# Kernel optimization log

Hardware: AMD Instinct MI355X
Metric: run time of the kernel (lower is better)

The kernel has to match this reference:

```python
import jax, jax.numpy as jnp
import numpy as np
from jax import lax

B, P, NB, NF, NC, R = 128, 2048, 2000, 250, 16, 128
LS = NB - NF  # number of simulated bins = len_bins_gensig - 1


def setup_inputs() -> dict:
    key = jax.random.key(0)
    ks = jax.random.split(key, 10)
    return {
        'batched_stim_spat': jax.random.normal(ks[0], (B, P), jnp.float32),
        'stim_time': jax.random.normal(ks[1], (NB,), jnp.float32),
        'batched_initial_spike_section': (jax.random.uniform(ks[2], (B, NF)) < 0.05).astype(jnp.float32),
        'batched_coupling_cells': (jax.random.uniform(ks[3], (B, NC, NB)) < 0.05).astype(jnp.float32),
        'spatial_filter': jax.random.normal(ks[4], (P,), jnp.float32) * 0.02,
        'spatial_bias': jnp.float32(-2.0),
        'stim_timecourse_filter': jax.random.normal(ks[5], (NF,), jnp.float32) * 0.1,
        'feedback_filter': jax.random.normal(ks[6], (NF,), jnp.float32) * 0.05 - 0.02,
        'coupling_filter': jax.random.normal(ks[7], (NC, NF), jnp.float32) * 0.05,
        'u': jax.random.uniform(ks[8], (LS, B, R), jnp.float32),
        'n_repeats': R,
    }


def _corr1d_valid(x, k):
    # torch F.conv1d is cross-correlation; lax conv is too (no kernel flip)
    # x: (n,), k: (m,) -> (n - m + 1,)
    out = lax.conv_general_dilated(x[None, None, :], k[None, None, :], (1,), 'VALID',
                                   dimension_numbers=('NCH', 'OIH', 'NCH'))
    return out[0, 0]


def reference(batched_stim_spat, stim_time, batched_initial_spike_section,
              batched_coupling_cells, spatial_filter, spatial_bias,
              stim_timecourse_filter, feedback_filter, coupling_filter, u, n_repeats):
    nf = stim_timecourse_filter.shape[0]

    # stimulus time component: (n_bins - nf + 1,)
    filt_time = _corr1d_valid(stim_time, stim_timecourse_filter)

    # spatial exp arg for separable linear-spatial GLM:
    # einsum('bpt,p->bt', stim_spat[:,:,None]*filt_time, spatial_filter)
    # factors into outer product of (stim_spat @ spatial_filter) and filt_time
    stim_gensig = (batched_stim_spat @ spatial_filter)[:, None] * filt_time[None, :] + spatial_bias  # (B, T)

    # coupling exp arg: conv1d over all coupled cells -> (B, T)
    coup = lax.conv_general_dilated(batched_coupling_cells, coupling_filter[None, :, :], (1,), 'VALID',
                                    dimension_numbers=('NCH', 'OIH', 'NCH'))[:, 0, :]

    gensig_piece = stim_gensig + coup  # (B, T) with T = n_bins - nf + 1
    len_sim = gensig_piece.shape[1] - 1

    # initial feedback window: last nf spike bins, broadcast over repeats
    batch = batched_stim_spat.shape[0]
    w0 = jnp.broadcast_to(batched_initial_spike_section[:, None, :], (batch, n_repeats, nf)) + 0.0

    def step(window, xs):
        g_t, u_t = xs  # (B,), (B, R)
        fb = jnp.einsum('brk,k->br', window, feedback_filter)
        g = g_t[:, None] + fb
        spike = (u_t < jax.nn.sigmoid(g)).astype(window.dtype)  # Bernoulli(sigmoid(g))
        window = jnp.concatenate([window[:, :, 1:], spike[:, :, None]], axis=2)
        return window, spike

    xs = (jnp.swapaxes(gensig_piece[:, :len_sim], 0, 1), u[:len_sim])  # ((LS,B), (LS,B,R))
    _, spikes = lax.scan(step, w0, xs)  # spikes: (LS, B, R)

    out = jnp.concatenate([w0, jnp.moveaxis(spikes, 0, 2)], axis=2)  # (B, R, n_bins)
    return out
```

## Files before the change

### kernel.cpp

```cpp
#include <hip/hip_runtime.h>
#include <math.h>

#define B_  128
#define P_  2048
#define NB_ 2000
#define NF_ 250
#define NC_ 16
#define R_  128
#define LS_ 1750
#define NT_ 1751
#define BR_ (B_ * R_)
#define H_  16
#define NBLK_ 110

typedef int v4i __attribute__((ext_vector_type(4)));

__device__ __forceinline__ unsigned csel32(unsigned a, unsigned b, unsigned long long m) {
    unsigned r;
    asm("v_cndmask_b32 %0, %1, %2, %3" : "=v"(r) : "v"(a), "v"(b), "s"(m));
    return r;
}

__device__ __forceinline__ double dsel2(double t, unsigned long long m) {
    long long tb = __double_as_longlong(t);
    int tlo = (int)tb, thi = (int)(tb >> 32);
    int rlo, rhi;
    asm("v_cndmask_b32 %0, 0, %2, %4\n\t"
        "v_cndmask_b32 %1, 0, %3, %4"
        : "=&v"(rlo), "=&v"(rhi)
        : "v"(tlo), "v"(thi), "s"(m));
    return __longlong_as_double(((long long)(unsigned)rlo) | ((long long)rhi << 32));
}

__device__ __forceinline__ double dand(double t, int m) {
    return __longlong_as_double(__double_as_longlong(t) & (long long)m);
}

__device__ __forceinline__ double fdiv_fast(double a, double b) {
    double r;
    asm("v_rcp_f64 %0, %1" : "=v"(r) : "v"(b));
    r = fma(fma(-b, r, 1.0), r, r);
    r = fma(fma(-b, r, 1.0), r, r);
    double q = a * r;
    q = fma(fma(-b, q, a), r, q);
    return q;
}

__device__ __forceinline__ double logit_fast(float uf) {
    double u = (double)uf;
    double v = 1.0 - u;
    double qd = fdiv_fast(u, v);
    long long bits = __double_as_longlong(qd);
    int e = (int)((bits >> 52) & 0x7FF) - 1023;
    double m = __longlong_as_double((bits & 0xFFFFFFFFFFFFFLL) | 0x3FF0000000000000LL);
    if (m > 1.4142135623730951) { m *= 0.5; e += 1; }
    double s = fdiv_fast(m - 1.0, m + 1.0);
    double z = s * s;
    double Q = fma(z, fma(z, fma(z, fma(z,
        0.09090909090909091, 0.1111111111111111),
        0.14285714285714285), 0.2), 0.3333333333333333);
    double logm = fma(2.0 * s, z * Q, 2.0 * s);
    return fma((double)e, 0.6931471805599453, logm);
}

__global__ __launch_bounds__(256) void k_pre(const float* __restrict__ st,
                                             const float* __restrict__ stf,
                                             const float* __restrict__ sp,
                                             const float* __restrict__ sf,
                                             double* __restrict__ ft,
                                             double* __restrict__ sdot) {
    if (blockIdx.x < 7) {
        int t = blockIdx.x * 256 + threadIdx.x;
        if (t >= NT_) return;
        double s = 0.0;
        for (int k = 0; k < NF_; ++k) s += (double)st[t + k] * (double)stf[k];
        ft[t] = s;
    } else {
        __shared__ double red[256];
        int b = blockIdx.x - 7;
        double s = 0.0;
        for (int p = threadIdx.x; p < P_; p += 256)
            s += (double)sp[(size_t)b * P_ + p] * (double)sf[p];
        red[threadIdx.x] = s;
        __syncthreads();
        for (int off = 128; off > 0; off >>= 1) {
            if (threadIdx.x < off) red[threadIdx.x] += red[threadIdx.x + off];
            __syncthreads();
        }
        if (threadIdx.x == 0) sdot[b] = red[0];
    }
}

__global__ __launch_bounds__(256) void k_coup(const float* __restrict__ cc,
                                              const float* __restrict__ cf,
                                              const double* __restrict__ sdot,
                                              const double* __restrict__ ft,
                                              const float* __restrict__ bias,
                                              double* __restrict__ gensig) {
    __shared__ __align__(16) float  ccs[NC_ * 512];
    __shared__ __align__(16) double cfs[NC_ * 256];
    __shared__ double red[3][64][4];
    int b = blockIdx.y, t0 = blockIdx.x * 256;
    int tid = threadIdx.x, lane = tid & 63, wv = tid >> 6;

    for (int idx = tid; idx < NC_ * 128; idx += 256) {
        int c = idx >> 7, j4 = (idx & 127) * 4, src = t0 + j4;
        const float* p = cc + ((size_t)b * NC_ + c) * NB_ + src;
        float4 v;
        if (src + 3 < NB_) v = *(const float4*)p;
        else {
            v.x = (src     < NB_) ? p[0] : 0.f;
            v.y = (src + 1 < NB_) ? p[1] : 0.f;
            v.z = (src + 2 < NB_) ? p[2] : 0.f;
            v.w = (src + 3 < NB_) ? p[3] : 0.f;
        }
        *(float4*)&ccs[c * 512 + j4] = v;
    }
    for (int idx = tid; idx < NC_ * 256; idx += 256) {
        int c = idx >> 8, k = idx & 255;
        cfs[idx] = (k < NF_) ? (double)cf[c * NF_ + k] : 0.0;
    }
    __syncthreads();

    double a0 = 0, a1 = 0, a2 = 0, a3 = 0;
    int base = lane * 4;
    for (int c = wv; c < NC_; c += 4) {
        const float*  row  = &ccs[c * 512];
        const double* crow = &cfs[c * 256];
        float4 cur = *(const float4*)&row[base];
        for (int k4 = 0; k4 < 252; k4 += 4) {
            float4 nxt = *(const float4*)&row[base + k4 + 4];
            double e0 = cur.x, e1 = cur.y, e2 = cur.z, e3 = cur.w;
            double e4 = nxt.x, e5 = nxt.y, e6 = nxt.z;
            double c0 = crow[k4], c1 = crow[k4 + 1], c2 = crow[k4 + 2], c3 = crow[k4 + 3];
            a0 += e0 * c0 + e1 * c1 + e2 * c2 + e3 * c3;
            a1 += e1 * c0 + e2 * c1 + e3 * c2 + e4 * c3;
            a2 += e2 * c0 + e3 * c1 + e4 * c2 + e5 * c3;
            a3 += e3 * c0 + e4 * c1 + e5 * c2 + e6 * c3;
            cur = nxt;
        }
    }
    if (wv > 0) {
        red[wv - 1][lane][0] = a0; red[wv - 1][lane][1] = a1;
        red[wv - 1][lane][2] = a2; red[wv - 1][lane][3] = a3;
    }
    __syncthreads();
    if (wv == 0) {
        a0 += red[0][lane][0] + red[1][lane][0] + red[2][lane][0];
        a1 += red[0][lane][1] + red[1][lane][1] + red[2][lane][1];
        a2 += red[0][lane][2] + red[1][lane][2] + red[2][lane][2];
        a3 += red[0][lane][3] + red[1][lane][3] + red[2][lane][3];
        double gb = (double)bias[0];
        double sd = sdot[b];
        double accs[4] = {a0, a1, a2, a3};
        int tb = t0 + base;
        for (int i = 0; i < 4; ++i) {
            int t = tb + i;
            if (t < LS_) gensig[(size_t)b * LS_ + t] = sd * ft[t] + gb + accs[i];
        }
    }
}

__global__ __launch_bounds__(512, 2) void k_scan(const double* __restrict__ gensig,
                                                 const float* __restrict__ u,
                                                 const float* __restrict__ iss,
                                                 const float* __restrict__ ff,
                                                 float* __restrict__ out) {
    __shared__ double farT_all[4][16 * 17];
    __shared__ double luring[2][4][4 * 64];
    int tid = threadIdx.x;
    int wv = tid >> 6, l = tid & 63;
    int swv = wv & 3;
    const bool isPrep = (wv >= 4);
    int gw = blockIdx.x * 4 + swv;
    int b = gw >> 3, rbase = (gw & 7) * 16;
    double* farT = &farT_all[swv][0];

    int lw = l & 15;
    int q  = l >> 4;
    int cn = l >> 2;
    int j  = l & 3;
    int jo = 16 + j;

    const unsigned long long COL0_ = 0x1111111111111111ull;
    const unsigned long long COL1_ = COL0_ << 1;
    const unsigned long long COL2_ = COL0_ << 2;
    const unsigned long long COL3_ = COL0_ << 3;
    const unsigned long long COL01_ = COL0_ | COL1_;

    const double* gs   = gensig + (size_t)b * LS_;
    const float*  up   = u + b * R_ + rbase + cn;
    float*        op   = out + ((size_t)(b * R_ + rbase + cn)) * NB_ + NF_;
    const float*  issb = iss + b * NF_;

    unsigned long long W0 = 0, W1 = 0, W2 = 0, W3 = 0;
    v4i Bf[4][6];
    double T1d = 0, T2d = 0, T3d = 0, T4d = 0, T5d = 0, T6d = 0;
    double tp7 = 0, tp8 = 0, tp9 = 0, tp10 = 0, tp11 = 0, tp12 = 0, tp13 = 0, tp14 = 0;
    double tp15 = 0;
    double thr0 = 0, thr1 = 0, thr2 = 0, thr3 = 0;
    double gprep = 0.0;
    float ur0 = 0.f, ur1 = 0.f, ur2 = 0.f, ur3 = 0.f;

    if (!isPrep) {
        for (int idx = l; idx < 16 * NF_; idx += 64) {
            int c = idx / NF_, k = idx - c * NF_;
            out[((size_t)(b * R_ + rbase + c)) * NB_ + k] = issb[k];
        }
        for (int k = 0; k < NF_; ++k) {
            unsigned long long bit = (issb[k] > 0.5f) ? 1ull : 0ull;
            if      (k <  64) W0 |= bit << k;
            else if (k < 128) W1 |= bit << (k - 64);
            else if (k < 192) W2 |= bit << (k - 128);
            else              W3 |= bit << (k - 192);
        }
        int Bword[4][6][4];
#pragma unroll
        for (int kc = 0; kc < 4; ++kc)
#pragma unroll
            for (int p = 0; p < 6; ++p)
#pragma unroll
                for (int w = 0; w < 4; ++w) Bword[kc][p][w] = 0;
#pragma unroll
        for (int kc = 0; kc < 4; ++kc) {
#pragma unroll
            for (int jj = 0; jj < 16; ++jj) {
                int k = kc * 64 + q * 16 + jj;
                int idx = k - lw;
                long long v = 0;
                if (idx >= 0 && idx < NF_)
                    v = __double2ll_rn((double)ff[idx] * 281474976710656.0);
#pragma unroll
                for (int p = 0; p < 6; ++p) {
                    int d = (int)((v + 128) & 255) - 128;
                    v = (v - (long long)d) >> 8;
                    Bword[kc][p][jj >> 2] |= (d & 255) << ((jj & 3) * 8);
                }
            }
        }
#pragma unroll
        for (int kc = 0; kc < 4; ++kc)
#pragma unroll
            for (int p = 0; p < 6; ++p) {
                v4i t; t.x = Bword[kc][p][0]; t.y = Bword[kc][p][1];
                t.z = Bword[kc][p][2]; t.w = Bword[kc][p][3];
                Bf[kc][p] = t;
            }
        T1d  = (double)ff[249]; T2d  = (double)ff[248]; T3d  = (double)ff[247];
        T4d  = (double)ff[246]; T5d  = (double)ff[245]; T6d  = (double)ff[244];
        tp7  = (double)ff[243]; tp8  = (double)ff[242]; tp9  = (double)ff[241];
        tp10 = (double)ff[240]; tp11 = (double)ff[239]; tp12 = (double)ff[238];
        tp13 = (double)ff[237]; tp14 = (double)ff[236]; tp15 = (double)ff[235];
    } else {
        ur0 = up[(size_t)(0  + j) * BR_];
        ur1 = up[(size_t)(4  + j) * BR_];
        ur2 = up[(size_t)(8  + j) * BR_];
        ur3 = up[(size_t)(12 + j) * BR_];
        luring[0][swv][  0 + l] = logit_fast(ur0);
        luring[0][swv][ 64 + l] = logit_fast(ur1);
        luring[0][swv][128 + l] = logit_fast(ur2);
        luring[0][swv][192 + l] = logit_fast(ur3);
        ur0 = up[(size_t)(16 + j) * BR_];
        ur1 = up[(size_t)(20 + j) * BR_];
        ur2 = up[(size_t)(24 + j) * BR_];
        ur3 = up[(size_t)(28 + j) * BR_];
        luring[1][swv][  0 + l] = logit_fast(ur0);
        luring[1][swv][ 64 + l] = logit_fast(ur1);
        luring[1][swv][128 + l] = logit_fast(ur2);
        luring[1][swv][192 + l] = logit_fast(ur3);
        ur0 = up[(size_t)(32 + j) * BR_];
        ur1 = up[(size_t)(36 + j) * BR_];
        ur2 = up[(size_t)(40 + j) * BR_];
        ur3 = up[(size_t)(44 + j) * BR_];
    }

    auto do_far = [&](double gp) {
        unsigned long long Sarr[4] = {W0, W1, W2, W3};
        v4i accm[6];
#pragma unroll
        for (int p = 0; p < 6; ++p) accm[p] = (v4i){0, 0, 0, 0};
#pragma unroll
        for (int kc = 0; kc < 4; ++kc) {
            unsigned f = (unsigned)((Sarr[kc] >> (q * 16)) & 0xFFFFull);
            v4i av;
            av.x = (int)((((f      ) & 0xFu) * 0x00204081u) & 0x01010101u);
            av.y = (int)((((f >>  4) & 0xFu) * 0x00204081u) & 0x01010101u);
            av.z = (int)((((f >>  8) & 0xFu) * 0x00204081u) & 0x01010101u);
            av.w = (int)((((f >> 12) & 0xFu) * 0x00204081u) & 0x01010101u);
#pragma unroll
            for (int p = 0; p < 6; ++p)
                accm[p] = __builtin_amdgcn_mfma_i32_16x16x64_i8(av, Bf[kc][p], accm[p], 0, 0, 0);
        }
#pragma unroll
        for (int r = 0; r < 4; ++r) {
            int lo = accm[0][r] + accm[1][r] * 256 + accm[2][r] * 65536;
            int hi = accm[3][r] + accm[4][r] * 256 + accm[5][r] * 65536;
            double fb = gp + (double)lo * 0x1p-48 + (double)hi * 0x1p-24;
            farT[(q * 4 + r) * 17 + lw] = fb;
        }
    };

    auto xbcalc = [&](int e4, unsigned qsnap) -> double {
        unsigned qs = qsnap >> e4;
        double x = (dand(tp7,  __builtin_amdgcn_sbfe((int)qs, jo - 7,  1)) +
                    dand(tp8,  __builtin_amdgcn_sbfe((int)qs, jo - 8,  1))) +
                   (dand(tp9,  __builtin_amdgcn_sbfe((int)qs, jo - 9,  1)) +
                    dand(tp10, __builtin_amdgcn_sbfe((int)qs, jo - 10, 1)));
        double y = (dand(tp11, __builtin_amdgcn_sbfe((int)qs, jo - 11, 1)) +
                    dand(tp12, __builtin_amdgcn_sbfe((int)qs, jo - 12, 1))) +
                   (dand(tp13, __builtin_amdgcn_sbfe((int)qs, jo - 13, 1)) +
                    dand(tp14, __builtin_amdgcn_sbfe((int)qs, jo - 14, 1)));
        return (x + y) + dand(tp15, __builtin_amdgcn_sbfe((int)qs, jo - 15, 1));
    };

    __syncthreads();

    if (!isPrep) {
        gprep = gs[lw];
        do_far(gprep);
        double lu0 = luring[0][swv][  0 + l];
        double lu1 = luring[0][swv][ 64 + l];
        double lu2 = luring[0][swv][128 + l];
        double lu3 = luring[0][swv][192 + l];
        __asm__ volatile("s_waitcnt lgkmcnt(0)" ::: "memory");
        thr0 = lu0 - farT[cn * 17 +  0 + j];
        thr1 = lu1 - farT[cn * 17 +  4 + j];
        thr2 = lu2 - farT[cn * 17 +  8 + j];
        thr3 = lu3 - farT[cn * 17 + 12 + j];
        { int tg = 16 + lw; if (tg > LS_ - 1) tg = LS_ - 1; gprep = gs[tg]; }
    }

    __syncthreads();

#define ROUND(E, XB, THR) { \
    double d4 = dsel2(T4d, A4); \
    double d5 = dsel2(T5d, A5); \
    double d6 = dsel2(T6d, A6); \
    double xb0 = (XB) + ((d4 + d5) + d6); \
    double xb1 = xb0 + T1d; \
    double xc0 = xb0 + T2d, xc1 = xb1 + T2d; \
    double xd0 = xb0 + T3d, xd1 = xb1 + T3d, xd2 = xc0 + T3d, xd3 = xc1 + T3d; \
    unsigned long long Bm0 = __ballot(xb0 > (THR)); \
    unsigned long long Bm1 = __ballot(xb1 > (THR)); \
    unsigned long long Bm2 = __ballot(xc0 > (THR)); \
    unsigned long long Bm3 = __ballot(xc1 > (THR)); \
    unsigned long long Bm4 = __ballot(xd0 > (THR)); \
    unsigned long long Bm5 = __ballot(xd1 > (THR)); \
    unsigned long long Bm6 = __ballot(xd2 > (THR)); \
    unsigned long long Bm7 = __ballot(xd3 > (THR)); \
    unsigned long long a3p = P >> 1, a2p = P >> 2; \
    unsigned long long C0 = Bm0 ^ (a3p & (Bm4 ^ Bm0)); \
    unsigned long long C1 = Bm1 ^ (a3p & (Bm5 ^ Bm1)); \
    unsigned long long C2 = Bm2 ^ (a3p & (Bm6 ^ Bm2)); \
    unsigned long long C3 = Bm3 ^ (a3p & (Bm7 ^ Bm3)); \
    unsigned long long D0 = C0 ^ (a2p & (C2 ^ C0)); \
    unsigned long long D1 = C1 ^ (a2p & (C3 ^ C1)); \
    unsigned long long Dd = D1 ^ D0; \
    unsigned long long S = (D0 ^ ((P >> 3) & Dd)) & COL0_; \
    S |= (D0 ^ ((S << 1) & Dd)) & COL1_; \
    { unsigned long long a2s = S << 2; \
      unsigned long long D0b = C0 ^ (a2s & (C2 ^ C0)); \
      unsigned long long D1b = C1 ^ (a2s & (C3 ^ C1)); \
      S |= (D0b ^ ((S << 1) & (D1b ^ D0b))) & COL2_; } \
    { unsigned long long a3s = S << 3, a2s = S << 2; \
      unsigned long long C0c = Bm0 ^ (a3s & (Bm4 ^ Bm0)); \
      unsigned long long C1c = Bm1 ^ (a3s & (Bm5 ^ Bm1)); \
      unsigned long long C2c = Bm2 ^ (a3s & (Bm6 ^ Bm2)); \
      unsigned long long C3c = Bm3 ^ (a3s & (Bm7 ^ Bm3)); \
      unsigned long long D0c = C0c ^ (a2s & (C2c ^ C0c)); \
      unsigned long long D1c = C1c ^ (a2s & (C3c ^ C1c)); \
      S |= (D0c ^ ((S << 1) & (D1c ^ D0c))) & COL3_; } \
    unsigned long long mm; \
    mm = S & COL0_;        mm |= mm << 1; mm |= mm << 2; \
    QL = csel32(QL, QL | (1u << (16 + 4 * (E) + 0)), mm); \
    mm = (S >> 1) & COL0_; mm |= mm << 1; mm |= mm << 2; \
    QL = csel32(QL, QL | (1u << (16 + 4 * (E) + 1)), mm); \
    mm = (S >> 2) & COL0_; mm |= mm << 1; mm |= mm << 2; \
    QL = csel32(QL, QL | (1u << (16 + 4 * (E) + 2)), mm); \
    mm = (S >> 3) & COL0_; mm |= mm << 1; mm |= mm << 2; \
    QL = csel32(QL, QL | (1u << (16 + 4 * (E) + 3)), mm); \
    A4 = S; \
    A5 = ((S << 1) & ~COL0_) | ((P >> 3) & COL0_); \
    A6 = ((S << 2) & ~COL01_) | ((P >> 2) & COL01_); \
    P = S; \
}

    int blk = 0;
    for (int t0 = 0; t0 < LS_; t0 += H_, ++blk) {
        if (!isPrep) {
            unsigned QL = 0;
            unsigned long long P = 0, A4 = 0, A5 = 0, A6 = 0;
            double XB1, XB2, XB3;
            ROUND(0, 0.0, thr0)
            XB1 = xbcalc(4, QL);
            ROUND(1, XB1, thr1)
            XB2 = xbcalc(8, QL);
            ROUND(2, XB2, thr2)
            XB3 = xbcalc(12, QL);
            ROUND(3, XB3, thr3)
            unsigned q2 = QL >> 16;

            int rem = LS_ - t0; if (rem > H_) rem = H_;
            int s0 = 4 * j;
            if (s0 + 3 < rem) {
                float4 o;
                o.x = (float)((q2 >> (s0    )) & 1u);
                o.y = (float)((q2 >> (s0 + 1)) & 1u);
                o.z = (float)((q2 >> (s0 + 2)) & 1u);
                o.w = (float)((q2 >> (s0 + 3)) & 1u);
                *(float4*)(op + t0 + s0) = o;
            } else {
#pragma unroll
                for (int e = 0; e < 4; ++e)
                    if (s0 + e < rem) op[t0 + s0 + e] = (float)((q2 >> (s0 + e)) & 1u);
            }

            if (t0 + H_ < LS_) {
                double lu0 = luring[(blk + 1) & 1][swv][  0 + l];
                double lu1 = luring[(blk + 1) & 1][swv][ 64 + l];
                double lu2 = luring[(blk + 1) & 1][swv][128 + l];
                double lu3 = luring[(blk + 1) & 1][swv][192 + l];

                int q2i = __builtin_amdgcn_ds_bpermute(lw << 4, (int)q2);
                unsigned long long q2n = (unsigned long long)(unsigned)q2i;
                W0 = (W0 >> 16) | (W1 << 48);
                W1 = (W1 >> 16) | (W2 << 48);
                W2 = (W2 >> 16) | (W3 << 48);
                W3 = (W3 >> 16) | (q2n << 42);

                do_far(gprep);
                __asm__ volatile("s_waitcnt lgkmcnt(0)" ::: "memory");
                thr0 = lu0 - farT[cn * 17 +  0 + j];
                thr1 = lu1 - farT[cn * 17 +  4 + j];
                thr2 = lu2 - farT[cn * 17 +  8 + j];
                thr3 = lu3 - farT[cn * 17 + 12 + j];

                int tg = t0 + 32 + lw; if (tg > LS_ - 1) tg = LS_ - 1;
                gprep = gs[tg];
            }
        } else {
            if (blk <= NBLK_ - 3) {
                double lu0 = logit_fast(ur0), lu1 = logit_fast(ur1);
                double lu2 = logit_fast(ur2), lu3 = logit_fast(ur3);
                luring[blk & 1][swv][  0 + l] = lu0;
                luring[blk & 1][swv][ 64 + l] = lu1;
                luring[blk & 1][swv][128 + l] = lu2;
                luring[blk & 1][swv][192 + l] = lu3;
                if (blk <= NBLK_ - 4) {
                    int T = (blk + 3) * H_;
                    int t_;
                    t_ = T +  0 + j; if (t_ > LS_ - 1) t_ = LS_ - 1; ur0 = up[(size_t)t_ * BR_];
                    t_ = T +  4 + j; if (t_ > LS_ - 1) t_ = LS_ - 1; ur1 = up[(size_t)t_ * BR_];
                    t_ = T +  8 + j; if (t_ > LS_ - 1) t_ = LS_ - 1; ur2 = up[(size_t)t_ * BR_];
                    t_ = T + 12 + j; if (t_ > LS_ - 1) t_ = LS_ - 1; ur3 = up[(size_t)t_ * BR_];
                }
            }
        }
        __syncthreads();
    }
#undef ROUND
}

extern "C" void kernel_launch(void* const* d_in, const int* in_sizes, int n_in,
                              void* d_out, int out_size, void* d_ws, size_t ws_size,
                              hipStream_t stream) {
    const float* stim_spat = (const float*)d_in[0];
    const float* stim_time = (const float*)d_in[1];
    const float* iss       = (const float*)d_in[2];
    const float* cc        = (const float*)d_in[3];
    const float* sf        = (const float*)d_in[4];
    const float* bias      = (const float*)d_in[5];
    const float* stf       = (const float*)d_in[6];
    const float* ff        = (const float*)d_in[7];
    const float* cf        = (const float*)d_in[8];
    const float* u         = (const float*)d_in[9];
    (void)in_sizes; (void)n_in; (void)out_size; (void)ws_size;

    float* out = (float*)d_out;

    double* ws     = (double*)d_ws;
    double* gensig = ws;
    double* ft     = gensig + (size_t)B_ * LS_;
    double* sdot   = ft + NT_;

    k_pre  <<<135, 256, 0, stream>>>(stim_time, stf, stim_spat, sf, ft, sdot);
    k_coup <<<dim3(7, B_), 256, 0, stream>>>(cc, cf, sdot, ft, bias, gensig);
    k_scan <<<B_ * 2, 512, 0, stream>>>(gensig, u, iss, ff, out);
}
```

Before: 524.6 us.

## Overlap far-feedback MFMA with spike rounds, precompute subset sums, cheapen logit

Splits the far-feedback matrix product so the MFMA work on already-known window bits is issued before the serial spike rounds, leaving only a small correction MFMA for the newly produced bits afterwards. The rounds now select precomputed subset sums of the near-feedback taps through a mux tree and compare them against a threshold minus the selection, instead of adding taps per candidate. The logit preparation also drops Newton iterations and evaluates its polynomial in float. These aim to shorten the critical path of the sequential recurrence, at the cost of more registers and lower precision in the logit, which may flip borderline Bernoulli decisions.

```diff
diff --git a/kernel.cpp b/kernel.cpp
--- a/kernel.cpp
+++ b/kernel.cpp
@@ -21,14 +21,13 @@
     return r;
 }
 
-__device__ __forceinline__ double dsel2(double t, unsigned long long m) {
-    long long tb = __double_as_longlong(t);
-    int tlo = (int)tb, thi = (int)(tb >> 32);
+__device__ __forceinline__ double dsel_ab(double a, double b, unsigned long long m) {
+    long long ab = __double_as_longlong(a), bb = __double_as_longlong(b);
     int rlo, rhi;
-    asm("v_cndmask_b32 %0, 0, %2, %4\n\t"
-        "v_cndmask_b32 %1, 0, %3, %4"
+    asm("v_cndmask_b32 %0, %2, %4, %6\n\t"
+        "v_cndmask_b32 %1, %3, %5, %6"
         : "=&v"(rlo), "=&v"(rhi)
-        : "v"(tlo), "v"(thi), "s"(m));
+        : "v"((int)ab), "v"((int)(ab >> 32)), "v"((int)bb), "v"((int)(bb >> 32)), "s"(m));
     return __longlong_as_double(((long long)(unsigned)rlo) | ((long long)rhi << 32));
 }
 
@@ -36,30 +35,27 @@
     return __longlong_as_double(__double_as_longlong(t) & (long long)m);
 }
 
-__device__ __forceinline__ double fdiv_fast(double a, double b) {
+__device__ __forceinline__ double rcp1(double b) {
     double r;
     asm("v_rcp_f64 %0, %1" : "=v"(r) : "v"(b));
     r = fma(fma(-b, r, 1.0), r, r);
-    r = fma(fma(-b, r, 1.0), r, r);
-    double q = a * r;
-    q = fma(fma(-b, q, a), r, q);
-    return q;
+    return r;
 }
 
 __device__ __forceinline__ double logit_fast(float uf) {
     double u = (double)uf;
     double v = 1.0 - u;
-    double qd = fdiv_fast(u, v);
+    double qd = u * rcp1(v);
     long long bits = __double_as_longlong(qd);
     int e = (int)((bits >> 52) & 0x7FF) - 1023;
     double m = __longlong_as_double((bits & 0xFFFFFFFFFFFFFLL) | 0x3FF0000000000000LL);
     if (m > 1.4142135623730951) { m *= 0.5; e += 1; }
-    double s = fdiv_fast(m - 1.0, m + 1.0);
-    double z = s * s;
-    double Q = fma(z, fma(z, fma(z, fma(z,
-        0.09090909090909091, 0.1111111111111111),
-        0.14285714285714285), 0.2), 0.3333333333333333);
-    double logm = fma(2.0 * s, z * Q, 2.0 * s);
+    double s = (m - 1.0) * rcp1(m + 1.0);
+    float zf = (float)(s * s);
+    float Qf = fmaf(zf, fmaf(zf, fmaf(zf, fmaf(zf,
+        0.09090909090909091f, 0.1111111111111111f),
+        0.14285714285714285f), 0.2f), 0.3333333333333333f);
+    double logm = fma(2.0 * s, (double)(zf * Qf), 2.0 * s);
     return fma((double)e, 0.6931471805599453, logm);
 }
 
@@ -198,6 +194,8 @@
     double T1d = 0, T2d = 0, T3d = 0, T4d = 0, T5d = 0, T6d = 0;
     double tp7 = 0, tp8 = 0, tp9 = 0, tp10 = 0, tp11 = 0, tp12 = 0, tp13 = 0, tp14 = 0;
     double tp15 = 0;
+    double SC1 = 0, SC2 = 0, SC3 = 0, SC4 = 0, SC5 = 0, SC6 = 0, SC7 = 0;
+    double Cc0 = 0, Cc1 = 0, Cc2 = 0, Cc3 = 0, Cc4 = 0, Cc5 = 0, Cc6 = 0, Cc7 = 0;
     double thr0 = 0, thr1 = 0, thr2 = 0, thr3 = 0;
     double gprep = 0.0;
     float ur0 = 0.f, ur1 = 0.f, ur2 = 0.f, ur3 = 0.f;
@@ -251,6 +249,10 @@
         tp7  = (double)ff[243]; tp8  = (double)ff[242]; tp9  = (double)ff[241];
         tp10 = (double)ff[240]; tp11 = (double)ff[239]; tp12 = (double)ff[238];
         tp13 = (double)ff[237]; tp14 = (double)ff[236]; tp15 = (double)ff[235];
+        SC1 = T1d; SC2 = T2d; SC3 = T1d + T2d;
+        SC4 = T3d; SC5 = T3d + T1d; SC6 = T3d + T2d; SC7 = (T3d + T2d) + T1d;
+        Cc0 = 0.0; Cc1 = T4d; Cc2 = T5d; Cc3 = T4d + T5d;
+        Cc4 = T6d; Cc5 = T6d + T4d; Cc6 = T6d + T5d; Cc7 = (T6d + T5d) + T4d;
     } else {
         ur0 = up[(size_t)(0  + j) * BR_];
         ur1 = up[(size_t)(4  + j) * BR_];
@@ -332,22 +334,23 @@
 
     __syncthreads();
 
-#define ROUND(E, XB, THR) { \
-    double d4 = dsel2(T4d, A4); \
-    double d5 = dsel2(T5d, A5); \
-    double d6 = dsel2(T6d, A6); \
-    double xb0 = (XB) + ((d4 + d5) + d6); \
-    double xb1 = xb0 + T1d; \
-    double xc0 = xb0 + T2d, xc1 = xb1 + T2d; \
-    double xd0 = xb0 + T3d, xd1 = xb1 + T3d, xd2 = xc0 + T3d, xd3 = xc1 + T3d; \
-    unsigned long long Bm0 = __ballot(xb0 > (THR)); \
-    unsigned long long Bm1 = __ballot(xb1 > (THR)); \
-    unsigned long long Bm2 = __ballot(xc0 > (THR)); \
-    unsigned long long Bm3 = __ballot(xc1 > (THR)); \
-    unsigned long long Bm4 = __ballot(xd0 > (THR)); \
-    unsigned long long Bm5 = __ballot(xd1 > (THR)); \
-    unsigned long long Bm6 = __ballot(xd2 > (THR)); \
-    unsigned long long Bm7 = __ballot(xd3 > (THR)); \
+#define ROUND(E, PRE2) { \
+    double u0 = dsel_ab(Cc0, Cc1, A4); \
+    double u1 = dsel_ab(Cc2, Cc3, A4); \
+    double u2 = dsel_ab(Cc4, Cc5, A4); \
+    double u3 = dsel_ab(Cc6, Cc7, A4); \
+    double v0 = dsel_ab(u0, u1, A5); \
+    double v1 = dsel_ab(u2, u3, A5); \
+    double sel = dsel_ab(v0, v1, A6); \
+    double rhs = (PRE2) - sel; \
+    unsigned long long Bm0 = __ballot(0.0 > rhs); \
+    unsigned long long Bm1 = __ballot(SC1 > rhs); \
+    unsigned long long Bm2 = __ballot(SC2 > rhs); \
+    unsigned long long Bm3 = __ballot(SC3 > rhs); \
+    unsigned long long Bm4 = __ballot(SC4 > rhs); \
+    unsigned long long Bm5 = __ballot(SC5 > rhs); \
+    unsigned long long Bm6 = __ballot(SC6 > rhs); \
+    unsigned long long Bm7 = __ballot(SC7 > rhs); \
     unsigned long long a3p = P >> 1, a2p = P >> 2; \
     unsigned long long C0 = Bm0 ^ (a3p & (Bm4 ^ Bm0)); \
     unsigned long long C1 = Bm1 ^ (a3p & (Bm5 ^ Bm1)); \
@@ -388,17 +391,42 @@
     int blk = 0;
     for (int t0 = 0; t0 < LS_; t0 += H_, ++blk) {
         if (!isPrep) {
+            bool more = (t0 + H_ < LS_);
+            unsigned long long Ws0 = (W0 >> 16) | (W1 << 48);
+            unsigned long long Ws1 = (W1 >> 16) | (W2 << 48);
+            unsigned long long Ws2 = (W2 >> 16) | (W3 << 48);
+            unsigned long long Ws3 = (W3 >> 16);
+            v4i accm[6];
+#pragma unroll
+            for (int p = 0; p < 6; ++p) accm[p] = (v4i){0, 0, 0, 0};
+            if (more) {
+                unsigned long long Sarr[4] = {Ws0, Ws1, Ws2, Ws3};
+#pragma unroll
+                for (int kc = 0; kc < 4; ++kc) {
+                    unsigned f = (unsigned)((Sarr[kc] >> (q * 16)) & 0xFFFFull);
+                    v4i av;
+                    av.x = (int)((((f      ) & 0xFu) * 0x00204081u) & 0x01010101u);
+                    av.y = (int)((((f >>  4) & 0xFu) * 0x00204081u) & 0x01010101u);
+                    av.z = (int)((((f >>  8) & 0xFu) * 0x00204081u) & 0x01010101u);
+                    av.w = (int)((((f >> 12) & 0xFu) * 0x00204081u) & 0x01010101u);
+#pragma unroll
+                    for (int p = 0; p < 6; ++p)
+                        accm[p] = __builtin_amdgcn_mfma_i32_16x16x64_i8(av, Bf[kc][p], accm[p], 0, 0, 0);
+                }
+            }
+
             unsigned QL = 0;
             unsigned long long P = 0, A4 = 0, A5 = 0, A6 = 0;
-            double XB1, XB2, XB3;
-            ROUND(0, 0.0, thr0)
-            XB1 = xbcalc(4, QL);
-            ROUND(1, XB1, thr1)
-            XB2 = xbcalc(8, QL);
-            ROUND(2, XB2, thr2)
-            XB3 = xbcalc(12, QL);
-            ROUND(3, XB3, thr3)
+            ROUND(0, thr0)
+            double pre21 = thr1 - xbcalc(4, QL);
+            ROUND(1, pre21)
+            double pre22 = thr2 - xbcalc(8, QL);
+            ROUND(2, pre22)
+            double pre23 = thr3 - xbcalc(12, QL);
+            ROUND(3, pre23)
             unsigned q2 = QL >> 16;
+
+            int q2i = __builtin_amdgcn_ds_bpermute(lw << 4, (int)q2);
 
             int rem = LS_ - t0; if (rem > H_) rem = H_;
             int s0 = 4 * j;
@@ -415,25 +443,38 @@
                     if (s0 + e < rem) op[t0 + s0 + e] = (float)((q2 >> (s0 + e)) & 1u);
             }
 
-            if (t0 + H_ < LS_) {
+            if (more) {
                 double lu0 = luring[(blk + 1) & 1][swv][  0 + l];
                 double lu1 = luring[(blk + 1) & 1][swv][ 64 + l];
                 double lu2 = luring[(blk + 1) & 1][swv][128 + l];
                 double lu3 = luring[(blk + 1) & 1][swv][192 + l];
 
-                int q2i = __builtin_amdgcn_ds_bpermute(lw << 4, (int)q2);
                 unsigned long long q2n = (unsigned long long)(unsigned)q2i;
-                W0 = (W0 >> 16) | (W1 << 48);
-                W1 = (W1 >> 16) | (W2 << 48);
-                W2 = (W2 >> 16) | (W3 << 48);
-                W3 = (W3 >> 16) | (q2n << 42);
-
-                do_far(gprep);
+                unsigned long long W3d = q2n << 42;
+                unsigned fd = (unsigned)((W3d >> (q * 16)) & 0xFFFFull);
+                v4i avd;
+                avd.x = (int)((((fd      ) & 0xFu) * 0x00204081u) & 0x01010101u);
+                avd.y = (int)((((fd >>  4) & 0xFu) * 0x00204081u) & 0x01010101u);
+                avd.z = (int)((((fd >>  8) & 0xFu) * 0x00204081u) & 0x01010101u);
+                avd.w = (int)((((fd >> 12) & 0xFu) * 0x00204081u) & 0x01010101u);
+#pragma unroll
+                for (int p = 0; p < 6; ++p)
+                    accm[p] = __builtin_amdgcn_mfma_i32_16x16x64_i8(avd, Bf[3][p], accm[p], 0, 0, 0);
+
+#pragma unroll
+                for (int r = 0; r < 4; ++r) {
+                    int lo = accm[0][r] + accm[1][r] * 256 + accm[2][r] * 65536;
+                    int hi = accm[3][r] + accm[4][r] * 256 + accm[5][r] * 65536;
+                    double fb = gprep + (double)lo * 0x1p-48 + (double)hi * 0x1p-24;
+                    farT[(q * 4 + r) * 17 + lw] = fb;
+                }
                 __asm__ volatile("s_waitcnt lgkmcnt(0)" ::: "memory");
                 thr0 = lu0 - farT[cn * 17 +  0 + j];
                 thr1 = lu1 - farT[cn * 17 +  4 + j];
                 thr2 = lu2 - farT[cn * 17 +  8 + j];
                 thr3 = lu3 - farT[cn * 17 + 12 + j];
+
+                W0 = Ws0; W1 = Ws1; W2 = Ws2; W3 = Ws3 | W3d;
 
                 int tg = t0 + 32 + lw; if (tg > LS_ - 1) tg = LS_ - 1;
                 gprep = gs[tg];
```

Result: no change. 527.1 us (+0.5%).
